# Optimization experiments

Measured on AMD Instinct MI355X. Metric: run time of the kernel, lower is better.

Reference implementation:

```python
import jax, jax.numpy as jnp
import numpy as np

C = 64
C8 = C // 8
C16 = C // 16


def setup_inputs() -> dict:
    key = jax.random.key(0)
    ks = jax.random.split(key, 11)
    s = lambda fan_in: 1.0 / np.sqrt(fan_in)
    return {
        "x": jax.random.normal(ks[0], (4, C, 64, 64), dtype=jnp.float32),
        # 1x1 convs == per-pixel linear: weight [out, in], bias [out]
        "Wq": jax.random.uniform(ks[1], (C8, C), minval=-s(C), maxval=s(C)),
        "bq": jax.random.uniform(ks[2], (C8,), minval=-s(C), maxval=s(C)),
        "Wk": jax.random.uniform(ks[3], (C8, C), minval=-s(C), maxval=s(C)),
        "bk": jax.random.uniform(ks[4], (C8,), minval=-s(C), maxval=s(C)),
        "Wv": jax.random.uniform(ks[5], (C, C), minval=-s(C), maxval=s(C)),
        "bv": jax.random.uniform(ks[6], (C,), minval=-s(C), maxval=s(C)),
        "W1": jax.random.uniform(ks[7], (C16, C), minval=-s(C), maxval=s(C)),
        "b1": jax.random.uniform(ks[8], (C16,), minval=-s(C), maxval=s(C)),
        "W2": jax.random.uniform(ks[9], (C, C16), minval=-s(C16), maxval=s(C16)),
        "b2": jax.random.uniform(ks[10], (C,), minval=-s(C16), maxval=s(C16)),
    }


def reference(x, Wq, bq, Wk, bk, Wv, bv, W1, b1, W2, b2):
    b, c, h, w = x.shape
    n = h * w
    xf = x.reshape(b, c, n)                                   # [b,c,n]
    Q = jnp.einsum('qc,bcn->bnq', Wq, xf) + bq                # [b,n,c/8]
    K = jnp.einsum('kc,bcn->bkn', Wk, xf) + bk[None, :, None] # [b,c/8,n]
    V = jnp.einsum('vc,bcn->bvn', Wv, xf) + bv[None, :, None] # [b,c,n]
    scores = jnp.einsum('bnq,bqm->bnm', Q, K) / jnp.sqrt(jnp.float32(c))
    att = jax.nn.softmax(scores, axis=-1)                     # [b,n,n]
    # self_attention_map = V @ att^T
    sa = jnp.einsum('bvm,bnm->bvn', V, att).reshape(b, c, h, w)
    # SE-style channel gate
    avg = xf.mean(axis=2)                                     # [b,c]
    gate = jax.nn.sigmoid(jax.nn.relu(avg @ W1.T + b1) @ W2.T + b2)
    return sa * gate[:, :, None, None]
```

## Files before the change

### kernel.cpp

```cpp
#include <hip/hip_runtime.h>
#include <hip/hip_bf16.h>

typedef __attribute__((ext_vector_type(8))) short bf16x8;
typedef __attribute__((ext_vector_type(4))) float f32x4;
typedef __attribute__((ext_vector_type(4))) unsigned short u16x4;
typedef __attribute__((ext_vector_type(8))) unsigned short u16x8;

#define WS_QB 0
#define WS_KB 131072
#define WS_VB 262144
#define WS_AVG_U 1310720

__device__ __forceinline__ unsigned short bf_hi(float x) {
    __hip_bfloat16 h = __float2bfloat16(x);
    return *reinterpret_cast<unsigned short*>(&h);
}

__global__ __launch_bounds__(256) void qkv_kernel(
    const float* __restrict__ x,
    const float* __restrict__ Wq, const float* __restrict__ bq,
    const float* __restrict__ Wk, const float* __restrict__ bk,
    const float* __restrict__ Wv, const float* __restrict__ bv,
    unsigned short* __restrict__ Qb, unsigned short* __restrict__ Kb,
    unsigned short* __restrict__ Vb)
{
    const int bx = blockIdx.x;
    const int ntile = bx & 15;
    const int rg = (bx >> 4) % 10;
    const int b = bx / 160;
    const int n = (ntile << 8) + threadIdx.x;
    const float* xb = x + b * 262144;

    const float* W; const float* bias;
    if (rg == 0)      { W = Wq; bias = bq; }
    else if (rg == 1) { W = Wk; bias = bk; }
    else              { W = Wv + (rg - 2) * 8 * 64; bias = bv + (rg - 2) * 8; }

    float acc[8];
#pragma unroll
    for (int j = 0; j < 8; ++j) acc[j] = bias[j];

#pragma unroll 8
    for (int c = 0; c < 64; ++c) {
        const float xv = xb[c * 4096 + n];
#pragma unroll
        for (int j = 0; j < 8; ++j) acc[j] += W[j * 64 + c] * xv;
    }

    if (rg == 0) {
        unsigned short tmp[8];
#pragma unroll
        for (int j = 0; j < 8; ++j) tmp[j] = bf_hi(acc[j] * 0.125f);
        *(u16x8*)&Qb[(b * 4096 + n) * 8] = *(const u16x8*)tmp;
    } else if (rg == 1) {
        unsigned short tmp[8];
#pragma unroll
        for (int j = 0; j < 8; ++j) tmp[j] = bf_hi(acc[j]);
        *(u16x8*)&Kb[(b * 4096 + n) * 8] = *(const u16x8*)tmp;
    } else {
        const int r0 = (rg - 2) * 8;
#pragma unroll
        for (int j = 0; j < 8; ++j) Vb[(b * 64 + r0 + j) * 4096 + n] = bf_hi(acc[j]);
    }
}

__global__ __launch_bounds__(256) void avg_kernel(
    const float* __restrict__ x, float* __restrict__ avg)
{
    const int bc = blockIdx.x;
    const int t = threadIdx.x;
    const float* row = x + bc * 4096;
    float s = 0.0f;
#pragma unroll
    for (int k = 0; k < 4; ++k) {
        const float4 v = *(const float4*)&row[t * 16 + k * 4];
        s += (v.x + v.y) + (v.z + v.w);
    }
    for (int off = 32; off > 0; off >>= 1) s += __shfl_down(s, off);
    __shared__ float wsum[4];
    if ((t & 63) == 0) wsum[t >> 6] = s;
    __syncthreads();
    if (t == 0) avg[bc] = (wsum[0] + wsum[1] + wsum[2] + wsum[3]) * (1.0f / 4096.0f);
}

__global__ __launch_bounds__(512) void attn_kernel(
    const unsigned short* __restrict__ Qb, const unsigned short* __restrict__ Kb,
    const unsigned short* __restrict__ Vb, const float* __restrict__ avg,
    const float* __restrict__ W1, const float* __restrict__ b1,
    const float* __restrict__ W2, const float* __restrict__ b2,
    float* __restrict__ out)
{
    __shared__ __align__(16) unsigned short smem[24576];
    __shared__ float zls[64], zrec[64], gls[64], avgs[64];

    const int t = threadIdx.x;
    const int h = t >> 8;
    const int tt = t & 255;
    const int ws_ = (t >> 6) & 3;
    const int l = t & 63;
    const int g = l >> 4;
    const int l15 = l & 15;

    const int b = blockIdx.x >> 6;
    const int q0 = (blockIdx.x & 63) << 6;
    const int mbase = h << 11;

    unsigned short* VsH = smem + h * 8192;
    unsigned short* PsH = smem + 16384 + h * 4096;

    if (t < 64) { avgs[t] = avg[b * 64 + t]; zls[t] = 0.0f; }

    bf16x8 zf = {};
    bf16x8 qf[4];
#pragma unroll
    for (int qt = 0; qt < 4; ++qt) {
        bf16x8 v = *(const bf16x8*)&Qb[(b * 4096 + q0 + qt * 16 + l15) * 8];
        qf[qt] = (g == 0) ? v : zf;
    }

    const int srow = tt >> 2;
    const int scol = (tt & 3) * 16;
    const int ssw = (srow & 7) << 3;
    const unsigned short* vsrc = &Vb[(b * 64 + srow) * 4096 + mbase];

    {
        u16x8 a = *(const u16x8*)&vsrc[scol];
        u16x8 c = *(const u16x8*)&vsrc[scol + 8];
        *(u16x8*)&VsH[srow * 64 + (scol ^ ssw)] = a;
        *(u16x8*)&VsH[srow * 64 + ((scol + 8) ^ ssw)] = c;
    }
    const int mrow = ws_ * 16 + l15;
    bf16x8 kf_next;
    {
        bf16x8 kv = *(const bf16x8*)&Kb[(b * 4096 + mbase + mrow) * 8];
        kf_next = (g == 0) ? kv : zf;
    }

    f32x4 acc[4];
#pragma unroll
    for (int qt = 0; qt < 4; ++qt)
#pragma unroll
        for (int r = 0; r < 4; ++r) acc[qt][r] = 0.0f;
    float zreg[4] = {0.f, 0.f, 0.f, 0.f};
    const int vswz = ((ws_ * 16 + l15) & 7) << 3;

    for (int i = 0; i < 32; ++i) {
        __syncthreads();

        const int inx = (i < 31) ? i + 1 : 31;
        u16x8 va = *(const u16x8*)&vsrc[inx * 64 + scol];
        u16x8 vb2 = *(const u16x8*)&vsrc[inx * 64 + scol + 8];

        bf16x8 kf = kf_next;
        {
            bf16x8 kv = *(const bf16x8*)&Kb[(b * 4096 + mbase + inx * 64 + mrow) * 8];
            kf_next = (g == 0) ? kv : zf;
        }
        f32x4 dz;
#pragma unroll
        for (int r = 0; r < 4; ++r) dz[r] = 0.0f;
#pragma unroll
        for (int qt = 0; qt < 4; ++qt) {
            f32x4 d = __builtin_amdgcn_mfma_f32_16x16x32_bf16(kf, qf[qt], dz, 0, 0, 0);
            float p[4];
#pragma unroll
            for (int r = 0; r < 4; ++r) p[r] = __expf(d[r]);
            zreg[qt] += (p[0] + p[1]) + (p[2] + p[3]);
            u16x4 pw;
#pragma unroll
            for (int r = 0; r < 4; ++r) pw[r] = bf_hi(p[r]);
            const int q = qt * 16 + l15;
            const int col = ws_ * 16 + g * 4;
            *(u16x4*)&PsH[q * 64 + (col ^ ((q & 7) << 3))] = pw;
        }

        __syncthreads();

        {
            const int base = ((i + 1) & 1) * 4096 + srow * 64;
            *(u16x8*)&VsH[base + (scol ^ ssw)] = va;
            *(u16x8*)&VsH[base + ((scol + 8) ^ ssw)] = vb2;
        }

        {
            const int vbase = (i & 1) * 4096 + (ws_ * 16 + l15) * 64;
#pragma unroll
            for (int kcb = 0; kcb < 2; ++kcb) {
                const int colA = kcb * 32 + g * 8;
                const bf16x8 af = *(const bf16x8*)&VsH[vbase + (colA ^ vswz)];
#pragma unroll
                for (int qt = 0; qt < 4; ++qt) {
                    const int q = qt * 16 + l15;
                    const bf16x8 bfr = *(const bf16x8*)&PsH[q * 64 + (colA ^ ((q & 7) << 3))];
                    acc[qt] = __builtin_amdgcn_mfma_f32_16x16x32_bf16(af, bfr, acc[qt], 0, 0, 0);
                }
            }
        }
    }

    __syncthreads();

#pragma unroll
    for (int qt = 0; qt < 4; ++qt) {
        float z = zreg[qt];
        z += __shfl_xor(z, 16);
        z += __shfl_xor(z, 32);
        if (g == 0) atomicAdd(&zls[qt * 16 + l15], z);
    }
    if (t < 64) {
        float hreg[4];
#pragma unroll
        for (int j = 0; j < 4; ++j) {
            float hh = b1[j];
            for (int c = 0; c < 64; ++c) hh += W1[j * 64 + c] * avgs[c];
            hreg[j] = fmaxf(hh, 0.0f);
        }
        float gg = b2[t];
#pragma unroll
        for (int j = 0; j < 4; ++j) gg += W2[t * 4 + j] * hreg[j];
        gls[t] = 1.0f / (1.0f + __expf(-gg));
    }
    __syncthreads();

    if (t < 64) zrec[t] = 1.0f / zls[t];
    float* cpart = (float*)smem;
    if (h == 1) {
#pragma unroll
        for (int qt = 0; qt < 4; ++qt)
#pragma unroll
            for (int r = 0; r < 4; ++r)
                cpart[(ws_ * 16 + g * 4 + r) * 68 + qt * 16 + l15] = acc[qt][r];
    }
    __syncthreads();

    if (h == 0) {
#pragma unroll
        for (int qt = 0; qt < 4; ++qt) {
            const int q = qt * 16 + l15;
            const float rz = zrec[q];
#pragma unroll
            for (int r = 0; r < 4; ++r) {
                const int v = ws_ * 16 + g * 4 + r;
                const float val = acc[qt][r] + cpart[v * 68 + q];
                out[(b * 64 + v) * 4096 + q0 + q] = val * rz * gls[v];
            }
        }
    }
}

extern "C" void kernel_launch(void* const* d_in, const int* in_sizes, int n_in,
                              void* d_out, int out_size, void* d_ws, size_t ws_size,
                              hipStream_t stream) {
    const float* x  = (const float*)d_in[0];
    const float* Wq = (const float*)d_in[1];
    const float* bq = (const float*)d_in[2];
    const float* Wk = (const float*)d_in[3];
    const float* bk = (const float*)d_in[4];
    const float* Wv = (const float*)d_in[5];
    const float* bv = (const float*)d_in[6];
    const float* W1 = (const float*)d_in[7];
    const float* b1 = (const float*)d_in[8];
    const float* W2 = (const float*)d_in[9];
    const float* b2 = (const float*)d_in[10];

    unsigned short* wsu = (unsigned short*)d_ws;
    unsigned short* Qb = wsu + WS_QB;
    unsigned short* Kb = wsu + WS_KB;
    unsigned short* Vb = wsu + WS_VB;
    float* avg = (float*)(wsu + WS_AVG_U);
    float* out = (float*)d_out;

    qkv_kernel<<<640, 256, 0, stream>>>(x, Wq, bq, Wk, bk, Wv, bv, Qb, Kb, Vb);
    avg_kernel<<<256, 256, 0, stream>>>(x, avg);
    attn_kernel<<<256, 512, 0, stream>>>(Qb, Kb, Vb, avg, W1, b1, W2, b2, out);
}
```

Baseline: 115.7 us.

## Use MFMA for QKV projection, fuse channel mean, and resplit attention blocks

The projection kernel now stages bf16 weights in shared memory and computes Q/K/V with MFMA tiles instead of scalar FMAs. The channel-mean reduction is folded into it through atomics, which needs a memset of the accumulator beforehand. The attention kernel changes from 512-thread blocks that split keys across two halves and then combine partials to 256-thread blocks. Each of those handles 32 queries over all 64 key tiles, with an XCD-aware block remap. The aims are to cut redundant x reads, one kernel launch, and the cross-half reduction, at the cost of bf16 rounding of x and weights and a longer serial key loop per block.

```diff
diff --git a/kernel.cpp b/kernel.cpp
--- a/kernel.cpp
+++ b/kernel.cpp
@@ -16,151 +16,173 @@
     return *reinterpret_cast<unsigned short*>(&h);
 }
 
-__global__ __launch_bounds__(256) void qkv_kernel(
+__global__ __launch_bounds__(256) void proj_kernel(
     const float* __restrict__ x,
     const float* __restrict__ Wq, const float* __restrict__ bq,
     const float* __restrict__ Wk, const float* __restrict__ bk,
     const float* __restrict__ Wv, const float* __restrict__ bv,
     unsigned short* __restrict__ Qb, unsigned short* __restrict__ Kb,
-    unsigned short* __restrict__ Vb)
+    unsigned short* __restrict__ Vb, float* __restrict__ avg)
 {
-    const int bx = blockIdx.x;
-    const int ntile = bx & 15;
-    const int rg = (bx >> 4) % 10;
-    const int b = bx / 160;
-    const int n = (ntile << 8) + threadIdx.x;
+    __shared__ __align__(16) unsigned short Wls[80 * 72];
+
+    const int t = threadIdx.x;
+    const int w = t >> 6;
+    const int l = t & 63;
+    const int g = l >> 4;
+    const int l15 = l & 15;
+    const int b = blockIdx.x >> 6;
+    const int n0 = (blockIdx.x & 63) << 6;
+    const int n = n0 + w * 16 + l15;
     const float* xb = x + b * 262144;
 
-    const float* W; const float* bias;
-    if (rg == 0)      { W = Wq; bias = bq; }
-    else if (rg == 1) { W = Wk; bias = bk; }
-    else              { W = Wv + (rg - 2) * 8 * 64; bias = bv + (rg - 2) * 8; }
-
-    float acc[8];
-#pragma unroll
-    for (int j = 0; j < 8; ++j) acc[j] = bias[j];
-
-#pragma unroll 8
-    for (int c = 0; c < 64; ++c) {
-        const float xv = xb[c * 4096 + n];
-#pragma unroll
-        for (int j = 0; j < 8; ++j) acc[j] += W[j * 64 + c] * xv;
-    }
-
-    if (rg == 0) {
-        unsigned short tmp[8];
-#pragma unroll
-        for (int j = 0; j < 8; ++j) tmp[j] = bf_hi(acc[j] * 0.125f);
-        *(u16x8*)&Qb[(b * 4096 + n) * 8] = *(const u16x8*)tmp;
-    } else if (rg == 1) {
-        unsigned short tmp[8];
-#pragma unroll
-        for (int j = 0; j < 8; ++j) tmp[j] = bf_hi(acc[j]);
-        *(u16x8*)&Kb[(b * 4096 + n) * 8] = *(const u16x8*)tmp;
-    } else {
-        const int r0 = (rg - 2) * 8;
-#pragma unroll
-        for (int j = 0; j < 8; ++j) Vb[(b * 64 + r0 + j) * 4096 + n] = bf_hi(acc[j]);
-    }
-}
-
-__global__ __launch_bounds__(256) void avg_kernel(
-    const float* __restrict__ x, float* __restrict__ avg)
-{
-    const int bc = blockIdx.x;
-    const int t = threadIdx.x;
-    const float* row = x + bc * 4096;
-    float s = 0.0f;
-#pragma unroll
-    for (int k = 0; k < 4; ++k) {
-        const float4 v = *(const float4*)&row[t * 16 + k * 4];
-        s += (v.x + v.y) + (v.z + v.w);
-    }
-    for (int off = 32; off > 0; off >>= 1) s += __shfl_down(s, off);
-    __shared__ float wsum[4];
-    if ((t & 63) == 0) wsum[t >> 6] = s;
+    float xr[2][8];
+#pragma unroll
+    for (int kcb = 0; kcb < 2; ++kcb)
+#pragma unroll
+        for (int j = 0; j < 8; ++j)
+            xr[kcb][j] = xb[(kcb * 32 + g * 8 + j) * 4096 + n];
+
+#pragma unroll
+    for (int i = 0; i < 20; ++i) {
+        const int idx = i * 256 + t;
+        const int row = idx >> 6, col = idx & 63;
+        float wv;
+        if (row < 8)       wv = Wq[row * 64 + col];
+        else if (row < 16) wv = Wk[(row - 8) * 64 + col];
+        else               wv = Wv[(row - 16) * 64 + col];
+        Wls[row * 72 + col] = bf_hi(wv);
+    }
     __syncthreads();
-    if (t == 0) avg[bc] = (wsum[0] + wsum[1] + wsum[2] + wsum[3]) * (1.0f / 4096.0f);
-}
-
-__global__ __launch_bounds__(512) void attn_kernel(
+
+    bf16x8 bfr[2];
+#pragma unroll
+    for (int kcb = 0; kcb < 2; ++kcb)
+#pragma unroll
+        for (int j = 0; j < 8; ++j)
+            bfr[kcb][j] = (short)bf_hi(xr[kcb][j]);
+
+#pragma unroll
+    for (int tile = 0; tile < 5; ++tile) {
+        const bf16x8 a0 = *(const bf16x8*)&Wls[(tile * 16 + l15) * 72 + g * 8];
+        const bf16x8 a1 = *(const bf16x8*)&Wls[(tile * 16 + l15) * 72 + 32 + g * 8];
+        f32x4 acc;
+#pragma unroll
+        for (int r = 0; r < 4; ++r) acc[r] = 0.0f;
+        acc = __builtin_amdgcn_mfma_f32_16x16x32_bf16(a0, bfr[0], acc, 0, 0, 0);
+        acc = __builtin_amdgcn_mfma_f32_16x16x32_bf16(a1, bfr[1], acc, 0, 0, 0);
+
+        if (tile == 0) {
+            u16x4 ov;
+            if (g < 2) {
+#pragma unroll
+                for (int r = 0; r < 4; ++r) ov[r] = bf_hi((acc[r] + bq[g * 4 + r]) * 0.125f);
+                *(u16x4*)&Qb[(b * 4096 + n) * 8 + g * 4] = ov;
+            } else {
+#pragma unroll
+                for (int r = 0; r < 4; ++r) ov[r] = bf_hi(acc[r] + bk[(g - 2) * 4 + r]);
+                *(u16x4*)&Kb[(b * 4096 + n) * 8 + (g - 2) * 4] = ov;
+            }
+        } else {
+#pragma unroll
+            for (int r = 0; r < 4; ++r) {
+                const int v = (tile - 1) * 16 + g * 4 + r;
+                Vb[(b * 64 + v) * 4096 + n] = bf_hi(acc[r] + bv[v]);
+            }
+        }
+    }
+
+    {
+        const int c = t >> 2;
+        const float* xrow = xb + c * 4096 + n0 + ((t & 3) << 4);
+        float s = 0.0f;
+#pragma unroll
+        for (int k = 0; k < 4; ++k) {
+            const float4 v = *(const float4*)&xrow[k * 4];
+            s += (v.x + v.y) + (v.z + v.w);
+        }
+        s += __shfl_xor(s, 1);
+        s += __shfl_xor(s, 2);
+        if ((t & 3) == 0) atomicAdd(&avg[b * 64 + c], s * (1.0f / 4096.0f));
+    }
+}
+
+__global__ __launch_bounds__(256) void attn_kernel(
     const unsigned short* __restrict__ Qb, const unsigned short* __restrict__ Kb,
     const unsigned short* __restrict__ Vb, const float* __restrict__ avg,
     const float* __restrict__ W1, const float* __restrict__ b1,
     const float* __restrict__ W2, const float* __restrict__ b2,
     float* __restrict__ out)
 {
-    __shared__ __align__(16) unsigned short smem[24576];
-    __shared__ float zls[64], zrec[64], gls[64], avgs[64];
+    __shared__ __align__(16) unsigned short Vs[2][64][64];
+    __shared__ __align__(16) unsigned short Ps[32][64];
+    __shared__ float zls[32], gls[64], avgs[64];
 
     const int t = threadIdx.x;
-    const int h = t >> 8;
-    const int tt = t & 255;
-    const int ws_ = (t >> 6) & 3;
+    const int w = t >> 6;
     const int l = t & 63;
     const int g = l >> 4;
     const int l15 = l & 15;
 
-    const int b = blockIdx.x >> 6;
-    const int q0 = (blockIdx.x & 63) << 6;
-    const int mbase = h << 11;
-
-    unsigned short* VsH = smem + h * 8192;
-    unsigned short* PsH = smem + 16384 + h * 4096;
-
-    if (t < 64) { avgs[t] = avg[b * 64 + t]; zls[t] = 0.0f; }
+    const int wg = (blockIdx.x & 7) * 64 + (blockIdx.x >> 3);
+    const int b = wg >> 7;
+    const int q0 = (wg & 127) << 5;
+
+    if (t < 32) zls[t] = 0.0f;
+    if (t < 64) avgs[t] = avg[b * 64 + t];
 
     bf16x8 zf = {};
-    bf16x8 qf[4];
-#pragma unroll
-    for (int qt = 0; qt < 4; ++qt) {
+    bf16x8 qf[2];
+#pragma unroll
+    for (int qt = 0; qt < 2; ++qt) {
         bf16x8 v = *(const bf16x8*)&Qb[(b * 4096 + q0 + qt * 16 + l15) * 8];
         qf[qt] = (g == 0) ? v : zf;
     }
 
-    const int srow = tt >> 2;
-    const int scol = (tt & 3) * 16;
+    const int srow = t >> 2;
+    const int scol = (t & 3) << 4;
     const int ssw = (srow & 7) << 3;
-    const unsigned short* vsrc = &Vb[(b * 64 + srow) * 4096 + mbase];
+    const unsigned short* vsrc = &Vb[(b * 64 + srow) * 4096];
 
     {
         u16x8 a = *(const u16x8*)&vsrc[scol];
         u16x8 c = *(const u16x8*)&vsrc[scol + 8];
-        *(u16x8*)&VsH[srow * 64 + (scol ^ ssw)] = a;
-        *(u16x8*)&VsH[srow * 64 + ((scol + 8) ^ ssw)] = c;
-    }
-    const int mrow = ws_ * 16 + l15;
+        *(u16x8*)&Vs[0][srow][scol ^ ssw] = a;
+        *(u16x8*)&Vs[0][srow][(scol + 8) ^ ssw] = c;
+    }
+    const int mrow = w * 16 + l15;
     bf16x8 kf_next;
     {
-        bf16x8 kv = *(const bf16x8*)&Kb[(b * 4096 + mbase + mrow) * 8];
+        bf16x8 kv = *(const bf16x8*)&Kb[(b * 4096 + mrow) * 8];
         kf_next = (g == 0) ? kv : zf;
     }
 
-    f32x4 acc[4];
-#pragma unroll
-    for (int qt = 0; qt < 4; ++qt)
+    f32x4 acc[2];
+#pragma unroll
+    for (int qt = 0; qt < 2; ++qt)
 #pragma unroll
         for (int r = 0; r < 4; ++r) acc[qt][r] = 0.0f;
-    float zreg[4] = {0.f, 0.f, 0.f, 0.f};
-    const int vswz = ((ws_ * 16 + l15) & 7) << 3;
-
-    for (int i = 0; i < 32; ++i) {
+    float zreg[2] = {0.f, 0.f};
+    const int vsw = (l15 & 7) << 3;
+    const int psw = (l15 & 7) << 3;
+
+    for (int i = 0; i < 64; ++i) {
         __syncthreads();
 
-        const int inx = (i < 31) ? i + 1 : 31;
+        const int inx = (i < 63) ? i + 1 : 63;
         u16x8 va = *(const u16x8*)&vsrc[inx * 64 + scol];
         u16x8 vb2 = *(const u16x8*)&vsrc[inx * 64 + scol + 8];
 
         bf16x8 kf = kf_next;
         {
-            bf16x8 kv = *(const bf16x8*)&Kb[(b * 4096 + mbase + inx * 64 + mrow) * 8];
+            bf16x8 kv = *(const bf16x8*)&Kb[(b * 4096 + inx * 64 + mrow) * 8];
             kf_next = (g == 0) ? kv : zf;
         }
         f32x4 dz;
 #pragma unroll
         for (int r = 0; r < 4; ++r) dz[r] = 0.0f;
 #pragma unroll
-        for (int qt = 0; qt < 4; ++qt) {
+        for (int qt = 0; qt < 2; ++qt) {
             f32x4 d = __builtin_amdgcn_mfma_f32_16x16x32_bf16(kf, qf[qt], dz, 0, 0, 0);
             float p[4];
 #pragma unroll
@@ -170,38 +192,34 @@
 #pragma unroll
             for (int r = 0; r < 4; ++r) pw[r] = bf_hi(p[r]);
             const int q = qt * 16 + l15;
-            const int col = ws_ * 16 + g * 4;
-            *(u16x4*)&PsH[q * 64 + (col ^ ((q & 7) << 3))] = pw;
+            *(u16x4*)&Ps[q][(w * 16 + g * 4) ^ ((q & 7) << 3)] = pw;
         }
 
         __syncthreads();
 
         {
-            const int base = ((i + 1) & 1) * 4096 + srow * 64;
-            *(u16x8*)&VsH[base + (scol ^ ssw)] = va;
-            *(u16x8*)&VsH[base + ((scol + 8) ^ ssw)] = vb2;
+            unsigned short* dst = &Vs[(i + 1) & 1][srow][0];
+            *(u16x8*)&dst[scol ^ ssw] = va;
+            *(u16x8*)&dst[(scol + 8) ^ ssw] = vb2;
         }
 
         {
-            const int vbase = (i & 1) * 4096 + (ws_ * 16 + l15) * 64;
+            const unsigned short* vbuf = &Vs[i & 1][w * 16 + l15][0];
 #pragma unroll
             for (int kcb = 0; kcb < 2; ++kcb) {
                 const int colA = kcb * 32 + g * 8;
-                const bf16x8 af = *(const bf16x8*)&VsH[vbase + (colA ^ vswz)];
-#pragma unroll
-                for (int qt = 0; qt < 4; ++qt) {
-                    const int q = qt * 16 + l15;
-                    const bf16x8 bfr = *(const bf16x8*)&PsH[q * 64 + (colA ^ ((q & 7) << 3))];
+                const bf16x8 af = *(const bf16x8*)&vbuf[colA ^ vsw];
+#pragma unroll
+                for (int qt = 0; qt < 2; ++qt) {
+                    const bf16x8 bfr = *(const bf16x8*)&Ps[qt * 16 + l15][colA ^ psw];
                     acc[qt] = __builtin_amdgcn_mfma_f32_16x16x32_bf16(af, bfr, acc[qt], 0, 0, 0);
                 }
             }
         }
     }
 
-    __syncthreads();
-
-#pragma unroll
-    for (int qt = 0; qt < 4; ++qt) {
+#pragma unroll
+    for (int qt = 0; qt < 2; ++qt) {
         float z = zreg[qt];
         z += __shfl_xor(z, 16);
         z += __shfl_xor(z, 32);
@@ -222,28 +240,14 @@
     }
     __syncthreads();
 
-    if (t < 64) zrec[t] = 1.0f / zls[t];
-    float* cpart = (float*)smem;
-    if (h == 1) {
-#pragma unroll
-        for (int qt = 0; qt < 4; ++qt)
-#pragma unroll
-            for (int r = 0; r < 4; ++r)
-                cpart[(ws_ * 16 + g * 4 + r) * 68 + qt * 16 + l15] = acc[qt][r];
-    }
-    __syncthreads();
-
-    if (h == 0) {
-#pragma unroll
-        for (int qt = 0; qt < 4; ++qt) {
-            const int q = qt * 16 + l15;
-            const float rz = zrec[q];
-#pragma unroll
-            for (int r = 0; r < 4; ++r) {
-                const int v = ws_ * 16 + g * 4 + r;
-                const float val = acc[qt][r] + cpart[v * 68 + q];
-                out[(b * 64 + v) * 4096 + q0 + q] = val * rz * gls[v];
-            }
+#pragma unroll
+    for (int qt = 0; qt < 2; ++qt) {
+        const int q = qt * 16 + l15;
+        const float rz = 1.0f / zls[q];
+#pragma unroll
+        for (int r = 0; r < 4; ++r) {
+            const int v = w * 16 + g * 4 + r;
+            out[(b * 64 + v) * 4096 + q0 + q] = acc[qt][r] * rz * gls[v];
         }
     }
 }
@@ -270,7 +274,7 @@
     float* avg = (float*)(wsu + WS_AVG_U);
     float* out = (float*)d_out;
 
-    qkv_kernel<<<640, 256, 0, stream>>>(x, Wq, bq, Wk, bk, Wv, bv, Qb, Kb, Vb);
-    avg_kernel<<<256, 256, 0, stream>>>(x, avg);
-    attn_kernel<<<256, 512, 0, stream>>>(Qb, Kb, Vb, avg, W1, b1, W2, b2, out);
-}
+    hipMemsetAsync(avg, 0, 256 * sizeof(float), stream);
+    proj_kernel<<<256, 256, 0, stream>>>(x, Wq, bq, Wk, bk, Wv, bv, Qb, Kb, Vb, avg);
+    attn_kernel<<<512, 256, 0, stream>>>(Qb, Kb, Vb, avg, W1, b1, W2, b2, out);
+}
```

Measured after the change: 123.2 us. +6.5%, slower.
